# Kernel tuning notes

Measured on AMD Instinct MI355X. Metric: run time of the kernel, lower is better.

## Reference

```python
import jax, jax.numpy as jnp
import numpy as np

KH, KW, STRIDE, PAD, DIL = 3, 3, 1, 1, 1


def setup_inputs() -> dict:
    key = jax.random.key(0)
    ks = jax.random.split(key, 4)
    B, C, H, W, O = 4, 256, 64, 64, 256
    K = KH * KW
    x = jax.random.normal(ks[0], (B, C, H, W), jnp.float32)
    # offset/mask conv params (original inits to zero; use small random so offsets are non-trivial)
    w_om = jax.random.normal(ks[1], (3 * K, C, KH, KW), jnp.float32) * 0.01
    b_om = jnp.zeros((3 * K,), jnp.float32)
    # main weight: kaiming_uniform_(a=1) -> gain = sqrt(2/(1+1^2)) = 1, bound = sqrt(3)/sqrt(fan_in)
    fan_in = C * K
    bound = float(np.sqrt(3.0) / np.sqrt(fan_in))
    weight = jax.random.uniform(ks[2], (O, C, KH, KW), jnp.float32, -bound, bound)
    bias = jnp.zeros((O,), jnp.float32)
    return {"x": x, "w_om": w_om, "b_om": b_om, "weight": weight, "bias": bias}


def _deform_conv2d(x, offset, mask, weight, bias):
    # torchvision.ops.deform_conv2d semantics, deformable_groups=1, stride=1, pad=1, dil=1
    B, C, H, W = x.shape
    K = KH * KW
    # torchvision offset layout: per-tap interleaved (y, x) pairs along channel dim
    off_y = offset[:, 0::2]  # [B, K, H, W]
    off_x = offset[:, 1::2]  # [B, K, H, W]
    ky = (jnp.repeat(jnp.arange(KH), KW) * DIL).astype(x.dtype)  # [K]
    kx = (jnp.tile(jnp.arange(KW), KH) * DIL).astype(x.dtype)    # [K]
    base_y = (jnp.arange(H) * STRIDE - PAD).astype(x.dtype)
    base_x = (jnp.arange(W) * STRIDE - PAD).astype(x.dtype)
    py = base_y[None, None, :, None] + ky[None, :, None, None] + off_y  # [B,K,H,W]
    px = base_x[None, None, None, :] + kx[None, :, None, None] + off_x  # [B,K,H,W]
    y0 = jnp.floor(py)
    x0 = jnp.floor(px)
    ly = py - y0
    lx = px - x0
    y0i = y0.astype(jnp.int32)
    x0i = x0.astype(jnp.int32)
    x_flat = x.reshape(B, C, H * W)

    def gather(yy, xx):
        # zero-padded gather of one bilinear corner -> [B, C, K, H, W]
        valid = ((yy >= 0) & (yy < H) & (xx >= 0) & (xx < W)).astype(x.dtype)
        idx = (jnp.clip(yy, 0, H - 1) * W + jnp.clip(xx, 0, W - 1)).reshape(B, -1)
        g = jax.vmap(lambda xf, i: jnp.take(xf, i, axis=1))(x_flat, idx)
        return g.reshape(B, C, K, H, W) * valid.reshape(B, 1, K, H, W)

    w00 = ((1 - ly) * (1 - lx))[:, None]
    w01 = ((1 - ly) * lx)[:, None]
    w10 = (ly * (1 - lx))[:, None]
    w11 = (ly * lx)[:, None]
    val = (gather(y0i, x0i) * w00 + gather(y0i, x0i + 1) * w01
           + gather(y0i + 1, x0i) * w10 + gather(y0i + 1, x0i + 1) * w11)
    cols = val * mask[:, None]  # modulated columns [B,C,K,H,W]
    out = jnp.einsum('bckhw,ock->bohw', cols, weight.reshape(weight.shape[0], C, K))
    return out + bias[None, :, None, None]


def reference(x, w_om, b_om, weight, bias):
    om = jax.lax.conv_general_dilated(
        x, w_om, (STRIDE, STRIDE), ((PAD, PAD), (PAD, PAD)),
        rhs_dilation=(DIL, DIL), dimension_numbers=('NCHW', 'OIHW', 'NCHW'),
    ) + b_om[None, :, None, None]
    K = KH * KW
    o1, o2, m = om[:, :K], om[:, K:2 * K], om[:, 2 * K:]
    offset = jnp.concatenate([o1, o2], axis=1)  # [B, 2K, H, W]
    mask = jax.nn.sigmoid(m)                    # [B, K, H, W]
    return _deform_conv2d(x, offset, mask, weight, bias)
```

## Files before the change

### kernel.cpp

```cpp
#include <hip/hip_runtime.h>
#include <stdint.h>

#define B_ 4
#define C_ 256
#define H_ 64
#define W_ 64
#define O_ 256
#define K_ 9
#define CK 2304
#define HW 4096
#define NTOT 16384

typedef __bf16 bf16x8 __attribute__((ext_vector_type(8)));
typedef __bf16 bf16x4 __attribute__((ext_vector_type(4)));
typedef float f32x4 __attribute__((ext_vector_type(4)));
typedef float f32x2 __attribute__((ext_vector_type(2)));
typedef f32x2 __attribute__((aligned(4))) f32x2u;

__device__ __forceinline__ uint16_t f2bf(float f) {
  uint32_t u = __builtin_bit_cast(uint32_t, f);
  return (uint16_t)((u + 0x7FFFu + ((u >> 16) & 1u)) >> 16);
}

__device__ __forceinline__ uint32_t pk_bf16(float a, float b) {
  uint16_t lo = __builtin_bit_cast(uint16_t, (__bf16)a);
  uint16_t hi = __builtin_bit_cast(uint16_t, (__bf16)b);
  return (uint32_t)lo | ((uint32_t)hi << 16);
}

__global__ void kA_prep(const float* __restrict__ weight, const float* __restrict__ w_om,
                        const float* __restrict__ x, uint16_t* __restrict__ wb,
                        uint16_t* __restrict__ womb, uint16_t* __restrict__ xT) {
  int bx = blockIdx.x;
  int t = threadIdx.x;
  if (bx < 2304) {
    int idx = bx * 256 + t;
    int o = idx / CK;
    int rem = idx - o * CK;
    int k = rem >> 8, c = rem & 255;
    wb[idx] = f2bf(weight[(o * C_ + c) * K_ + k]);
  } else if (bx < 2592) {
    int idx = (bx - 2304) * 256 + t;
    int j = idx / CK;
    int ck = idx - j * CK;
    int k = ck >> 8, c = ck & 255;
    womb[idx] = (j < 27) ? f2bf(w_om[(j * 256 + c) * 9 + k]) : (uint16_t)0;
  } else {
    int bxl = bx - 2592;
    int ct = bxl & 3;
    int hwt = (bxl >> 2) & 63;
    int b = bxl >> 8;
    int l = t & 63;
    int cq = t >> 6;

    __shared__ __align__(16) uint16_t tile[64 * 72];

    const float* xb = x + ((b * 256 + ct * 64) * HW) + hwt * 64;
#pragma unroll
    for (int i = 0; i < 16; ++i) {
      int c = cq * 16 + i;
      tile[l * 72 + c] = f2bf(xb[c * HW + l]);
    }
    __syncthreads();

    int hw = t >> 2;
    int c8 = (t & 3) * 8;
    uint16_t* dst = xT + ((size_t)b << 20) + (size_t)(hwt * 64 + hw) * 256 + ct * 64;
    *(uint4*)&dst[c8] = *(const uint4*)&tile[hw * 72 + c8];
    *(uint4*)&dst[c8 + 32] = *(const uint4*)&tile[hw * 72 + c8 + 32];
  }
}

__device__ __forceinline__ void write_om(float v, int j, int n, const float* __restrict__ b_om,
                                         float* __restrict__ pypxmk) {
  if (j >= 27) return;
  float s = v + b_om[j];
  int b = n >> 12, hw = n & 4095;
  int h = hw >> 6, w = hw & 63;
  if (j < 18) {
    int k = j >> 1;
    int off = (b * 9 + k) * HW + hw;
    if ((j & 1) == 0)
      pypxmk[off] = (float)(h - 1 + k / 3) + s;
    else
      pypxmk[147456 + off] = (float)(w - 1 + k % 3) + s;
  } else {
    int k = j - 18;
    pypxmk[294912 + (b * 9 + k) * HW + hw] = 1.f / (1.f + __expf(-s));
  }
}

__global__ void k1_mfma(const uint16_t* __restrict__ womb, const uint16_t* __restrict__ xT,
                        const float* __restrict__ b_om, float* __restrict__ pypxmk) {
  int nt = blockIdx.x;
  int t = threadIdx.x;
  int lane = t & 63;
  int wid = t >> 6;
  int lr = lane & 15, q = lane >> 4;
  int n = nt * 64 + wid * 16 + lr;
  int b = n >> 12;
  int hw = n & 4095;
  int y = hw >> 6, xx = hw & 63;
  const uint16_t* xb = xT + ((size_t)b << 20);
  const uint16_t* zrow = womb + 31 * CK;

  f32x4 acc0 = {0.f, 0.f, 0.f, 0.f};
  f32x4 acc1 = {0.f, 0.f, 0.f, 0.f};

#pragma unroll
  for (int k = 0; k < 9; ++k) {
    int dy = k / 3, dx = k - dy * 3;
    int ny = y + dy - 1, nx = xx + dx - 1;
    bool valid = ((unsigned)ny < 64u) && ((unsigned)nx < 64u);
    int row = (min(max(ny, 0), 63) << 6) + min(max(nx, 0), 63);
    const uint16_t* bp = valid ? (xb + row * 256 + q * 8) : (zrow + q * 8);
    const uint16_t* ap = womb + lr * CK + k * 256 + q * 8;
#pragma unroll
    for (int kt = 0; kt < 8; ++kt) {
      int c0 = kt * 32;
      bf16x8 bF = *(const bf16x8*)&bp[c0];
      bf16x8 aF0 = *(const bf16x8*)&ap[c0];
      bf16x8 aF1 = *(const bf16x8*)&ap[16 * CK + c0];
      acc0 = __builtin_amdgcn_mfma_f32_16x16x32_bf16(aF0, bF, acc0, 0, 0, 0);
      acc1 = __builtin_amdgcn_mfma_f32_16x16x32_bf16(aF1, bF, acc1, 0, 0, 0);
    }
  }

#pragma unroll
  for (int r = 0; r < 4; ++r) {
    write_om(acc0[r], q * 4 + r, n, b_om, pypxmk);
    write_om(acc1[r], 16 + q * 4 + r, n, b_om, pypxmk);
  }
}

__global__ void k2_cols(const uint16_t* __restrict__ xT, const float* __restrict__ pypxmk,
                        uint16_t* __restrict__ cols) {
  int bx = blockIdx.x;
  int g = __builtin_amdgcn_readfirstlane(threadIdx.x >> 6);
  int lane = threadIdx.x & 63;

  const float* pyA = pypxmk;
  const float* pxA = pypxmk + 147456;
  const float* mkA = pypxmk + 294912;

  float py_c, px_c, mk_c;
  {
    int p = g;
    int pn = p / 9;
    int k = p - pn * 9;
    int n = (bx << 3) + pn;
    int poff = ((n >> 12) * 9 + k) * HW + (n & 4095);
    py_c = pyA[poff];
    px_c = pxA[poff];
    mk_c = mkA[poff];
  }

  for (int it = 0; it < 18; ++it) {
    int p = it * 4 + g;
    int pn = p / 9;
    int k = p - pn * 9;
    int n = (bx << 3) + pn;
    int b = n >> 12;

    float py = py_c, px = px_c, mk = mk_c;
    if (it < 17) {
      int p2 = (it + 1) * 4 + g;
      int pn2 = p2 / 9;
      int k2 = p2 - pn2 * 9;
      int n2 = (bx << 3) + pn2;
      int poff2 = ((n2 >> 12) * 9 + k2) * HW + (n2 & 4095);
      py_c = pyA[poff2];
      px_c = pxA[poff2];
      mk_c = mkA[poff2];
    }

    float fy0 = floorf(py), fx0 = floorf(px);
    float ly = py - fy0, lx = px - fx0;
    int y0 = (int)fy0, x0 = (int)fx0;
    bool vy0 = ((unsigned)y0 < 64u), vy1 = ((unsigned)(y0 + 1) < 64u);
    bool vx0 = ((unsigned)x0 < 64u), vx1 = ((unsigned)(x0 + 1) < 64u);
    float w00 = (vy0 && vx0) ? (1.f - ly) * (1.f - lx) * mk : 0.f;
    float w01 = (vy0 && vx1) ? (1.f - ly) * lx * mk : 0.f;
    float w10 = (vy1 && vx0) ? ly * (1.f - lx) * mk : 0.f;
    float w11 = (vy1 && vx1) ? ly * lx * mk : 0.f;
    bool sel0 = (x0 >= 63);
    bool sel1 = (x0 >= 0);
    float wa0 = (sel0 ? 0.f : w00) + (sel1 ? 0.f : w01);
    float wb0 = (sel0 ? w00 : 0.f) + (sel1 ? w01 : 0.f);
    float wa1 = (sel0 ? 0.f : w10) + (sel1 ? 0.f : w11);
    float wb1 = (sel0 ? w10 : 0.f) + (sel1 ? w11 : 0.f);
    int bx0 = min(max(x0, 0), 62);
    int a0 = min(max(y0, 0), 63) * 64 + bx0;
    int a1 = min(max(y0 + 1, 0), 63) * 64 + bx0;

    const uint16_t* xb = xT + ((size_t)b << 20);
    bf16x4 r00 = *(const bf16x4*)&xb[a0 * 256 + lane * 4];
    bf16x4 r01 = *(const bf16x4*)&xb[a0 * 256 + 256 + lane * 4];
    bf16x4 r10 = *(const bf16x4*)&xb[a1 * 256 + lane * 4];
    bf16x4 r11 = *(const bf16x4*)&xb[a1 * 256 + 256 + lane * 4];

    float v[4];
#pragma unroll
    for (int i = 0; i < 4; ++i)
      v[i] = wa0 * (float)r00[i] + wb0 * (float)r01[i] +
             wa1 * (float)r10[i] + wb1 * (float)r11[i];

    uint2 pk;
    pk.x = pk_bf16(v[0], v[1]);
    pk.y = pk_bf16(v[2], v[3]);
    *(uint2*)&cols[(size_t)n * CK + k * 256 + lane * 4] = pk;
  }
}

__global__ void k3_gemm(const uint16_t* __restrict__ wb, const uint16_t* __restrict__ cols,
                        const float* __restrict__ bias, float* __restrict__ out) {
  int bx = blockIdx.x;
  int mt = bx & 1;
  int nt = bx >> 1;
  int o0 = mt * 128;
  int n0 = nt * 64;
  int t = threadIdx.x;
  int lane = t & 63;
  int wid = t >> 6;
  int wm = wid >> 1, wn = wid & 1;
  int lr = lane & 15, q = lane >> 4;

  __shared__ __align__(16) uint16_t As[128 * 32];
  __shared__ __align__(16) uint16_t Bs[64 * 32];

  f32x4 acc[4][2];
  const f32x4 zero = {0.f, 0.f, 0.f, 0.f};
#pragma unroll
  for (int i = 0; i < 4; ++i)
#pragma unroll
    for (int j = 0; j < 2; ++j) acc[i][j] = zero;

  int r0 = t >> 2;
  int koff = (t & 3) * 8;
  const uint16_t* gA = wb + (o0 + r0) * CK + koff;
  const uint16_t* gB = cols + (n0 + r0) * CK + koff;

  for (int kt = 0; kt < 72; ++kt) {
    int k0 = kt * 32;
    __builtin_amdgcn_global_load_lds(
        (const __attribute__((address_space(1))) uint32_t*)(gA + k0),
        (__attribute__((address_space(3))) uint32_t*)&As[t * 8], 16, 0, 0);
    __builtin_amdgcn_global_load_lds(
        (const __attribute__((address_space(1))) uint32_t*)(gA + 64 * CK + k0),
        (__attribute__((address_space(3))) uint32_t*)&As[2048 + t * 8], 16, 0, 0);
    __builtin_amdgcn_global_load_lds(
        (const __attribute__((address_space(1))) uint32_t*)(gB + k0),
        (__attribute__((address_space(3))) uint32_t*)&Bs[t * 8], 16, 0, 0);
    __syncthreads();

    bf16x8 aF[4], bF[2];
#pragma unroll
    for (int i = 0; i < 4; ++i)
      aF[i] = *(const bf16x8*)&As[(wm * 64 + i * 16 + lr) * 32 + q * 8];
#pragma unroll
    for (int j = 0; j < 2; ++j)
      bF[j] = *(const bf16x8*)&Bs[(wn * 32 + j * 16 + lr) * 32 + q * 8];
#pragma unroll
    for (int i = 0; i < 4; ++i)
#pragma unroll
      for (int j = 0; j < 2; ++j)
        acc[i][j] = __builtin_amdgcn_mfma_f32_16x16x32_bf16(aF[i], bF[j], acc[i][j], 0, 0, 0);
    __syncthreads();
  }

  int bb = n0 >> 12;
  int hw0 = n0 & 4095;
#pragma unroll
  for (int i = 0; i < 4; ++i) {
#pragma unroll
    for (int r = 0; r < 4; ++r) {
      int o = o0 + wm * 64 + i * 16 + q * 4 + r;
      float bv = bias[o];
      float* orow = out + (bb * O_ + o) * HW + hw0;
#pragma unroll
      for (int j = 0; j < 2; ++j) orow[wn * 32 + j * 16 + lr] = acc[i][j][r] + bv;
    }
  }
}

__global__ void k0_wconv(const float* __restrict__ weight, uint16_t* __restrict__ wb) {
  int idx = blockIdx.x * 256 + threadIdx.x;
  if (idx >= O_ * CK) return;
  int o = idx / CK;
  int rem = idx - o * CK;
  int k = rem >> 8;
  int c = rem & 255;
  wb[idx] = f2bf(weight[(o * C_ + c) * K_ + k]);
}

__global__ void k1_offconv(const float* __restrict__ x, const float* __restrict__ w_om,
                           const float* __restrict__ b_om, float* __restrict__ pypxmk) {
  int bx = blockIdx.x;
  int jq = bx % 7;
  int h = (bx / 7) % H_;
  int b = bx / (7 * H_);
  int t = threadIdx.x;
  int w = t & 63;
  int cs = __builtin_amdgcn_readfirstlane(t >> 6);

  float acc[4] = {0.f, 0.f, 0.f, 0.f};
  const float* xb = x + (b * C_) * HW;

  for (int ci = 0; ci < 64; ++ci) {
    int c = cs * 64 + ci;
    const float* xr = xb + c * HW;
    float xv[3][3];
#pragma unroll
    for (int r = 0; r < 3; ++r) {
      int y = h - 1 + r;
      bool yv = ((unsigned)y < 64u);
#pragma unroll
      for (int dx = 0; dx < 3; ++dx) {
        int xx = w - 1 + dx;
        bool v = yv && ((unsigned)xx < 64u);
        xv[r][dx] = v ? xr[y * 64 + xx] : 0.f;
      }
    }
    const float* wp = w_om + ((jq * 4) * C_ + c) * 9;
#pragma unroll
    for (int jj = 0; jj < 4; ++jj) {
      int j = jq * 4 + jj;
      int jeff = (j < 27) ? jj : 0;
      const float* wj = wp + jeff * (C_ * 9);
      float a = 0.f;
#pragma unroll
      for (int r = 0; r < 3; ++r)
#pragma unroll
        for (int dx = 0; dx < 3; ++dx)
          a = fmaf(xv[r][dx], wj[r * 3 + dx], a);
      acc[jj] += a;
    }
  }

  __shared__ float red[4][4][64];
#pragma unroll
  for (int jj = 0; jj < 4; ++jj) red[cs][jj][w] = acc[jj];
  __syncthreads();

  int jj = t >> 6;
  int j = jq * 4 + jj;
  if (j < 27) {
    float s = red[0][jj][w] + red[1][jj][w] + red[2][jj][w] + red[3][jj][w] + b_om[j];
    float* pyA = pypxmk;
    float* pxA = pypxmk + 147456;
    float* mkA = pypxmk + 294912;
    if (j < 18) {
      int k = j >> 1;
      int off = (b * 9 + k) * HW + h * 64 + w;
      if ((j & 1) == 0)
        pyA[off] = (float)(h - 1 + k / 3) + s;
      else
        pxA[off] = (float)(w - 1 + k % 3) + s;
    } else {
      int k = j - 18;
      mkA[(b * 9 + k) * HW + h * 64 + w] = 1.f / (1.f + __expf(-s));
    }
  }
}

__global__ void k2_fb(const float* __restrict__ x, const float* __restrict__ pypxmk,
                      uint16_t* __restrict__ cols) {
  int bx = blockIdx.x;
  int cg = bx & 15;
  int h = (bx >> 4) & 63;
  int b = bx >> 10;
  int t = threadIdx.x;
  int w = t & 63;
  int g = t >> 6;

  const float* pyA = pypxmk;
  const float* pxA = pypxmk + 147456;
  const float* mkA = pypxmk + 294912;

  __shared__ uint16_t tile[64 * 146];
  const float* xb = x + b * C_ * HW;
  int cbase = cg * 16 + g * 4;

#pragma unroll
  for (int k = 0; k < 9; ++k) {
    int poff = (b * 9 + k) * HW + h * 64 + w;
    float py = pyA[poff];
    float px = pxA[poff];
    float mk = mkA[poff];
    float fy0 = floorf(py), fx0 = floorf(px);
    float ly = py - fy0, lx = px - fx0;
    int y0 = (int)fy0, x0 = (int)fx0;
    bool vy0 = ((unsigned)y0 < 64u), vy1 = ((unsigned)(y0 + 1) < 64u);
    bool vx0 = ((unsigned)x0 < 64u), vx1 = ((unsigned)(x0 + 1) < 64u);
    float w00 = (vy0 && vx0) ? (1.f - ly) * (1.f - lx) * mk : 0.f;
    float w01 = (vy0 && vx1) ? (1.f - ly) * lx * mk : 0.f;
    float w10 = (vy1 && vx0) ? ly * (1.f - lx) * mk : 0.f;
    float w11 = (vy1 && vx1) ? ly * lx * mk : 0.f;
    bool sel0 = (x0 >= 63);
    bool sel1 = (x0 >= 0);
    float wa0 = (sel0 ? 0.f : w00) + (sel1 ? 0.f : w01);
    float wb0 = (sel0 ? w00 : 0.f) + (sel1 ? w01 : 0.f);
    float wa1 = (sel0 ? 0.f : w10) + (sel1 ? 0.f : w11);
    float wb1 = (sel0 ? w10 : 0.f) + (sel1 ? w11 : 0.f);
    int bx0 = min(max(x0, 0), 62);
    int a0 = min(max(y0, 0), 63) * 64 + bx0;
    int a1 = min(max(y0 + 1, 0), 63) * 64 + bx0;

#pragma unroll
    for (int cp = 0; cp < 2; ++cp) {
      const float* xcA = xb + (cbase + cp * 2) * HW;
      const float* xcB = xcA + HW;
      f32x2 A0 = *(const f32x2u*)&xcA[a0];
      f32x2 A1 = *(const f32x2u*)&xcA[a1];
      f32x2 B0 = *(const f32x2u*)&xcB[a0];
      f32x2 B1 = *(const f32x2u*)&xcB[a1];
      float rA = wa0 * A0.x + wb0 * A0.y + wa1 * A1.x + wb1 * A1.y;
      float rB = wa0 * B0.x + wb0 * B0.y + wa1 * B1.x + wb1 * B1.y;
      *(uint32_t*)&tile[w * 146 + k * 16 + g * 4 + cp * 2] = pk_bf16(rA, rB);
    }
  }
  __syncthreads();

#pragma unroll
  for (int it = 0; it < 18; ++it) {
    int u = t + it * 256;
    int wu = u / 72;
    int rem = u - wu * 72;
    int k = rem >> 3;
    int cd = rem & 7;
    uint32_t val = *(const uint32_t*)&tile[wu * 146 + rem * 2];
    int n = b * HW + h * 64 + wu;
    int dst = n * CK + k * 256 + cg * 16 + cd * 2;
    *(uint32_t*)&cols[dst] = val;
  }
}

__global__ void k3_flex(const uint16_t* __restrict__ wb, const uint16_t* __restrict__ cols,
                        const float* __restrict__ bias, float* __restrict__ out) {
  int bx = blockIdx.x;
  int mt = bx & 1;
  int nt = bx >> 1;
  int o0 = mt * 128;
  int n0 = nt * 128;
  int t = threadIdx.x;
  int lane = t & 63;
  int wid = t >> 6;
  int wm = wid >> 1, wn = wid & 1;
  int lr = lane & 15, q = lane >> 4;

  __shared__ __align__(16) uint16_t As[128 * 32];
  __shared__ __align__(16) uint16_t Bs[128 * 32];

  f32x4 acc[4][4];
  const f32x4 zero = {0.f, 0.f, 0.f, 0.f};
#pragma unroll
  for (int i = 0; i < 4; ++i)
#pragma unroll
    for (int j = 0; j < 4; ++j) acc[i][j] = zero;

  int r0 = t >> 2;
  int koff = (t & 3) * 8;
  const uint16_t* gA = wb + (o0 + r0) * CK + koff;
  const uint16_t* gB = cols + (n0 + r0) * CK + koff;

  for (int kt = 0; kt < 72; ++kt) {
    int k0 = kt * 32;
    __builtin_amdgcn_global_load_lds(
        (const __attribute__((address_space(1))) uint32_t*)(gA + k0),
        (__attribute__((address_space(3))) uint32_t*)&As[t * 8], 16, 0, 0);
    __builtin_amdgcn_global_load_lds(
        (const __attribute__((address_space(1))) uint32_t*)(gA + 64 * CK + k0),
        (__attribute__((address_space(3))) uint32_t*)&As[2048 + t * 8], 16, 0, 0);
    __builtin_amdgcn_global_load_lds(
        (const __attribute__((address_space(1))) uint32_t*)(gB + k0),
        (__attribute__((address_space(3))) uint32_t*)&Bs[t * 8], 16, 0, 0);
    __builtin_amdgcn_global_load_lds(
        (const __attribute__((address_space(1))) uint32_t*)(gB + 64 * CK + k0),
        (__attribute__((address_space(3))) uint32_t*)&Bs[2048 + t * 8], 16, 0, 0);
    __syncthreads();

    bf16x8 aF[4], bF[4];
#pragma unroll
    for (int i = 0; i < 4; ++i)
      aF[i] = *(const bf16x8*)&As[(wm * 64 + i * 16 + lr) * 32 + q * 8];
#pragma unroll
    for (int j = 0; j < 4; ++j)
      bF[j] = *(const bf16x8*)&Bs[(wn * 64 + j * 16 + lr) * 32 + q * 8];
#pragma unroll
    for (int i = 0; i < 4; ++i)
#pragma unroll
      for (int j = 0; j < 4; ++j)
        acc[i][j] = __builtin_amdgcn_mfma_f32_16x16x32_bf16(aF[i], bF[j], acc[i][j], 0, 0, 0);
    __syncthreads();
  }

  int bb = n0 >> 12;
  int hw0 = n0 & 4095;
#pragma unroll
  for (int i = 0; i < 4; ++i) {
#pragma unroll
    for (int r = 0; r < 4; ++r) {
      int o = o0 + wm * 64 + i * 16 + q * 4 + r;
      float bv = bias[o];
      float* orow = out + (bb * O_ + o) * HW + hw0;
#pragma unroll
      for (int j = 0; j < 4; ++j) orow[wn * 64 + j * 16 + lr] = acc[i][j][r] + bv;
    }
  }
}

extern "C" void kernel_launch(void* const* d_in, const int* in_sizes, int n_in,
                              void* d_out, int out_size, void* d_ws, size_t ws_size,
                              hipStream_t stream) {
  const float* x = (const float*)d_in[0];
  const float* w_om = (const float*)d_in[1];
  const float* b_om = (const float*)d_in[2];
  const float* weight = (const float*)d_in[3];
  const float* bias = (const float*)d_in[4];
  float* out = (float*)d_out;

  char* ws = (char*)d_ws;
  uint16_t* wb = (uint16_t*)ws;
  uint16_t* womb = (uint16_t*)(ws + 1179648);
  uint16_t* xT = (uint16_t*)(ws + 1327104);
  float* pypxmk = (float*)(ws + 9715712);
  uint16_t* cols = (uint16_t*)(ws + 11485184);

  if (ws_size >= 86982656ull) {
    hipLaunchKernelGGL(kA_prep, dim3(3616), dim3(256), 0, stream, weight, w_om, x, wb, womb, xT);
    hipLaunchKernelGGL(k1_mfma, dim3(256), dim3(256), 0, stream, womb, xT, b_om, pypxmk);
    hipLaunchKernelGGL(k2_cols, dim3(2048), dim3(256), 0, stream, xT, pypxmk, cols);
    hipLaunchKernelGGL(k3_gemm, dim3(512), dim3(256), 0, stream, wb, cols, bias, out);
  } else {
    float* pypx_fb = (float*)(ws + 1179648);
    uint16_t* colsf = (uint16_t*)(ws + 2949120);
    hipLaunchKernelGGL(k0_wconv, dim3(2304), dim3(256), 0, stream, weight, wb);
    hipLaunchKernelGGL(k1_offconv, dim3(4 * 64 * 7), dim3(256), 0, stream, x, w_om, b_om, pypx_fb);
    hipLaunchKernelGGL(k2_fb, dim3(4 * 64 * 16), dim3(256), 0, stream, x, pypx_fb, colsf);
    hipLaunchKernelGGL(k3_flex, dim3(256), dim3(256), 0, stream, wb, colsf, bias, out);
  }
}
```

Measured before the change: 173.7 us.

## Fuse deformable gather into GEMM, building column tiles in LDS

Replaces the separate column-building kernel and GEMM with one fused kernel. Each block gathers bilinear-interpolated, mask-weighted columns for one kernel tap into an XOR-swizzled LDS slab, then runs MFMA over all 256 output channels while double-buffering weight tiles through LDS. This removes the write and re-read of the large bf16 column buffer in global memory and one launch. In exchange the gather is serialized with the MMA per tap, there are only 256 blocks of 512 threads, and the workspace threshold changes.

```diff
diff --git a/kernel.cpp b/kernel.cpp
--- a/kernel.cpp
+++ b/kernel.cpp
@@ -133,47 +133,24 @@
   }
 }
 
-__global__ void k2_cols(const uint16_t* __restrict__ xT, const float* __restrict__ pypxmk,
-                        uint16_t* __restrict__ cols) {
-  int bx = blockIdx.x;
-  int g = __builtin_amdgcn_readfirstlane(threadIdx.x >> 6);
-  int lane = threadIdx.x & 63;
-
-  const float* pyA = pypxmk;
-  const float* pxA = pypxmk + 147456;
-  const float* mkA = pypxmk + 294912;
-
-  float py_c, px_c, mk_c;
-  {
-    int p = g;
-    int pn = p / 9;
-    int k = p - pn * 9;
-    int n = (bx << 3) + pn;
-    int poff = ((n >> 12) * 9 + k) * HW + (n & 4095);
-    py_c = pyA[poff];
-    px_c = pxA[poff];
-    mk_c = mkA[poff];
-  }
-
-  for (int it = 0; it < 18; ++it) {
-    int p = it * 4 + g;
-    int pn = p / 9;
-    int k = p - pn * 9;
-    int n = (bx << 3) + pn;
-    int b = n >> 12;
-
-    float py = py_c, px = px_c, mk = mk_c;
-    if (it < 17) {
-      int p2 = (it + 1) * 4 + g;
-      int pn2 = p2 / 9;
-      int k2 = p2 - pn2 * 9;
-      int n2 = (bx << 3) + pn2;
-      int poff2 = ((n2 >> 12) * 9 + k2) * HW + (n2 & 4095);
-      py_c = pyA[poff2];
-      px_c = pxA[poff2];
-      mk_c = mkA[poff2];
-    }
-
+
+struct GatherState {
+  float wa0[4], wb0[4], wa1[4], wb1[4];
+  bf16x4 r00[4], r01[4], r10[4], r11[4];
+};
+
+__device__ __forceinline__ void gather_issue(GatherState& S, const uint16_t* __restrict__ xb,
+                                             const float* __restrict__ pyA,
+                                             const float* __restrict__ pxA,
+                                             const float* __restrict__ mkA,
+                                             int b, int kg, int n0, int rbase, int lane) {
+#pragma unroll
+  for (int j = 0; j < 4; ++j) {
+    int nrow = rbase + j;
+    int poff = (b * 9 + kg) * HW + ((n0 + nrow) & 4095);
+    float py = pyA[poff];
+    float px = pxA[poff];
+    float mk = mkA[poff];
     float fy0 = floorf(py), fx0 = floorf(px);
     float ly = py - fy0, lx = px - fx0;
     int y0 = (int)fy0, x0 = (int)fx0;
@@ -185,48 +162,99 @@
     float w11 = (vy1 && vx1) ? ly * lx * mk : 0.f;
     bool sel0 = (x0 >= 63);
     bool sel1 = (x0 >= 0);
-    float wa0 = (sel0 ? 0.f : w00) + (sel1 ? 0.f : w01);
-    float wb0 = (sel0 ? w00 : 0.f) + (sel1 ? w01 : 0.f);
-    float wa1 = (sel0 ? 0.f : w10) + (sel1 ? 0.f : w11);
-    float wb1 = (sel0 ? w10 : 0.f) + (sel1 ? w11 : 0.f);
+    S.wa0[j] = (sel0 ? 0.f : w00) + (sel1 ? 0.f : w01);
+    S.wb0[j] = (sel0 ? w00 : 0.f) + (sel1 ? w01 : 0.f);
+    S.wa1[j] = (sel0 ? 0.f : w10) + (sel1 ? 0.f : w11);
+    S.wb1[j] = (sel0 ? w10 : 0.f) + (sel1 ? w11 : 0.f);
     int bx0 = min(max(x0, 0), 62);
     int a0 = min(max(y0, 0), 63) * 64 + bx0;
     int a1 = min(max(y0 + 1, 0), 63) * 64 + bx0;
-
-    const uint16_t* xb = xT + ((size_t)b << 20);
-    bf16x4 r00 = *(const bf16x4*)&xb[a0 * 256 + lane * 4];
-    bf16x4 r01 = *(const bf16x4*)&xb[a0 * 256 + 256 + lane * 4];
-    bf16x4 r10 = *(const bf16x4*)&xb[a1 * 256 + lane * 4];
-    bf16x4 r11 = *(const bf16x4*)&xb[a1 * 256 + 256 + lane * 4];
-
+    S.r00[j] = *(const bf16x4*)&xb[a0 * 256 + lane * 4];
+    S.r01[j] = *(const bf16x4*)&xb[a0 * 256 + 256 + lane * 4];
+    S.r10[j] = *(const bf16x4*)&xb[a1 * 256 + lane * 4];
+    S.r11[j] = *(const bf16x4*)&xb[a1 * 256 + 256 + lane * 4];
+  }
+}
+
+__device__ __forceinline__ void gather_finish(const GatherState& S, uint16_t* bslab,
+                                              int rbase, int lane) {
+#pragma unroll
+  for (int j = 0; j < 4; ++j) {
+    int nrow = rbase + j;
     float v[4];
 #pragma unroll
     for (int i = 0; i < 4; ++i)
-      v[i] = wa0 * (float)r00[i] + wb0 * (float)r01[i] +
-             wa1 * (float)r10[i] + wb1 * (float)r11[i];
-
+      v[i] = S.wa0[j] * (float)S.r00[j][i] + S.wb0[j] * (float)S.r01[j][i] +
+             S.wa1[j] * (float)S.r10[j][i] + S.wb1[j] * (float)S.r11[j][i];
     uint2 pk;
     pk.x = pk_bf16(v[0], v[1]);
     pk.y = pk_bf16(v[2], v[3]);
-    *(uint2*)&cols[(size_t)n * CK + k * 256 + lane * 4] = pk;
-  }
-}
-
-__global__ void k3_gemm(const uint16_t* __restrict__ wb, const uint16_t* __restrict__ cols,
-                        const float* __restrict__ bias, float* __restrict__ out) {
-  int bx = blockIdx.x;
-  int mt = bx & 1;
-  int nt = bx >> 1;
-  int o0 = mt * 128;
-  int n0 = nt * 64;
+    int chunk = lane >> 1;
+    int chs = (chunk & 24) | ((chunk & 7) ^ (nrow & 7));
+    *(uint2*)&bslab[nrow * 256 + chs * 8 + (lane & 1) * 4] = pk;
+  }
+}
+
+__device__ __forceinline__ void stageA(const uint16_t* __restrict__ wb, uint16_t* asbuf,
+                                       int kbase, int t) {
+#pragma unroll
+  for (int i = 0; i < 4; ++i) {
+    int rr = i * 64 + (t >> 3);
+    const uint16_t* src = wb + rr * CK + kbase + (((t & 7) ^ (rr & 7)) << 3);
+    __builtin_amdgcn_global_load_lds(
+        (const __attribute__((address_space(1))) uint32_t*)src,
+        (__attribute__((address_space(3))) uint32_t*)&asbuf[i * 4096 + t * 8], 16, 0, 0);
+  }
+}
+
+__device__ __forceinline__ void mma_step(const uint16_t* AsP, const uint16_t* BsP,
+                                         f32x4 acc[4][2], int wm, int wn, int lr, int q,
+                                         int kt2) {
+#pragma unroll
+  for (int kc = 0; kc < 2; ++kc) {
+    bf16x8 aF[4], bF[2];
+#pragma unroll
+    for (int i = 0; i < 4; ++i) {
+      int row = wm * 64 + i * 16 + lr;
+      aF[i] = *(const bf16x8*)&AsP[row * 64 + (((kc * 4 + q) ^ (row & 7)) << 3)];
+    }
+#pragma unroll
+    for (int j = 0; j < 2; ++j) {
+      int row = wn * 32 + j * 16 + lr;
+      int kidx = kt2 * 8 + kc * 4 + q;
+      int chs = (kidx & 24) | ((kidx & 7) ^ (row & 7));
+      bF[j] = *(const bf16x8*)&BsP[row * 256 + chs * 8];
+    }
+#pragma unroll
+    for (int i = 0; i < 4; ++i)
+#pragma unroll
+      for (int j = 0; j < 2; ++j)
+        acc[i][j] = __builtin_amdgcn_mfma_f32_16x16x32_bf16(aF[i], bF[j], acc[i][j], 0, 0, 0);
+  }
+}
+
+__global__ __launch_bounds__(512, 2) void k23_fused(const uint16_t* __restrict__ wb,
+                                                    const uint16_t* __restrict__ xT,
+                                                    const float* __restrict__ pypxmk,
+                                                    const float* __restrict__ bias,
+                                                    float* __restrict__ out) {
+  __shared__ __align__(16) uint16_t As[2][16384];
+  __shared__ __align__(16) uint16_t Bs[16384];
+
   int t = threadIdx.x;
   int lane = t & 63;
-  int wid = t >> 6;
+  int wid = __builtin_amdgcn_readfirstlane(t >> 6);
+  int lr = lane & 15, q = lane >> 4;
   int wm = wid >> 1, wn = wid & 1;
-  int lr = lane & 15, q = lane >> 4;
-
-  __shared__ __align__(16) uint16_t As[128 * 32];
-  __shared__ __align__(16) uint16_t Bs[64 * 32];
+  int bx = blockIdx.x;
+  int swz = (bx & 7) * 32 + (bx >> 3);
+  int n0 = swz * 64;
+  int b = n0 >> 12;
+  int hw0 = n0 & 4095;
+  const uint16_t* xb = xT + ((size_t)b << 20);
+  const float* pyA = pypxmk;
+  const float* pxA = pypxmk + 147456;
+  const float* mkA = pypxmk + 294912;
 
   f32x4 acc[4][2];
   const f32x4 zero = {0.f, 0.f, 0.f, 0.f};
@@ -235,48 +263,41 @@
 #pragma unroll
     for (int j = 0; j < 2; ++j) acc[i][j] = zero;
 
-  int r0 = t >> 2;
-  int koff = (t & 3) * 8;
-  const uint16_t* gA = wb + (o0 + r0) * CK + koff;
-  const uint16_t* gB = cols + (n0 + r0) * CK + koff;
-
-  for (int kt = 0; kt < 72; ++kt) {
-    int k0 = kt * 32;
-    __builtin_amdgcn_global_load_lds(
-        (const __attribute__((address_space(1))) uint32_t*)(gA + k0),
-        (__attribute__((address_space(3))) uint32_t*)&As[t * 8], 16, 0, 0);
-    __builtin_amdgcn_global_load_lds(
-        (const __attribute__((address_space(1))) uint32_t*)(gA + 64 * CK + k0),
-        (__attribute__((address_space(3))) uint32_t*)&As[2048 + t * 8], 16, 0, 0);
-    __builtin_amdgcn_global_load_lds(
-        (const __attribute__((address_space(1))) uint32_t*)(gB + k0),
-        (__attribute__((address_space(3))) uint32_t*)&Bs[t * 8], 16, 0, 0);
-    __syncthreads();
-
-    bf16x8 aF[4], bF[2];
-#pragma unroll
-    for (int i = 0; i < 4; ++i)
-      aF[i] = *(const bf16x8*)&As[(wm * 64 + i * 16 + lr) * 32 + q * 8];
-#pragma unroll
-    for (int j = 0; j < 2; ++j)
-      bF[j] = *(const bf16x8*)&Bs[(wn * 32 + j * 16 + lr) * 32 + q * 8];
-#pragma unroll
-    for (int i = 0; i < 4; ++i)
-#pragma unroll
-      for (int j = 0; j < 2; ++j)
-        acc[i][j] = __builtin_amdgcn_mfma_f32_16x16x32_bf16(aF[i], bF[j], acc[i][j], 0, 0, 0);
-    __syncthreads();
-  }
-
-  int bb = n0 >> 12;
-  int hw0 = n0 & 4095;
+  GatherState S;
+  int wrow = wid * 8;
+
+  gather_issue(S, xb, pyA, pxA, mkA, b, 0, n0, wrow, lane);
+  gather_finish(S, Bs, wrow, lane);
+  gather_issue(S, xb, pyA, pxA, mkA, b, 0, n0, wrow + 4, lane);
+  gather_finish(S, Bs, wrow + 4, lane);
+  stageA(wb, As[0], 0, t);
+  __syncthreads();
+
+  for (int k = 0; k < 9; ++k) {
+    for (int kt2 = 0; kt2 < 4; ++kt2) {
+      if (!(k == 8 && kt2 == 3)) {
+        int kb2 = (kt2 == 3) ? (k + 1) * 256 : k * 256 + (kt2 + 1) * 64;
+        stageA(wb, As[(kt2 + 1) & 1], kb2, t);
+      }
+      mma_step(As[kt2 & 1], Bs, acc, wm, wn, lr, q, kt2);
+      __syncthreads();
+    }
+    if (k < 8) {
+      gather_issue(S, xb, pyA, pxA, mkA, b, k + 1, n0, wrow, lane);
+      gather_finish(S, Bs, wrow, lane);
+      gather_issue(S, xb, pyA, pxA, mkA, b, k + 1, n0, wrow + 4, lane);
+      gather_finish(S, Bs, wrow + 4, lane);
+      __syncthreads();
+    }
+  }
+
 #pragma unroll
   for (int i = 0; i < 4; ++i) {
 #pragma unroll
     for (int r = 0; r < 4; ++r) {
-      int o = o0 + wm * 64 + i * 16 + q * 4 + r;
+      int o = wm * 64 + i * 16 + q * 4 + r;
       float bv = bias[o];
-      float* orow = out + (bb * O_ + o) * HW + hw0;
+      float* orow = out + (b * O_ + o) * HW + hw0;
 #pragma unroll
       for (int j = 0; j < 2; ++j) orow[wn * 32 + j * 16 + lr] = acc[i][j][r] + bv;
     }
@@ -524,13 +545,11 @@
   uint16_t* womb = (uint16_t*)(ws + 1179648);
   uint16_t* xT = (uint16_t*)(ws + 1327104);
   float* pypxmk = (float*)(ws + 9715712);
-  uint16_t* cols = (uint16_t*)(ws + 11485184);
-
-  if (ws_size >= 86982656ull) {
+
+  if (ws_size >= 11485184ull) {
     hipLaunchKernelGGL(kA_prep, dim3(3616), dim3(256), 0, stream, weight, w_om, x, wb, womb, xT);
     hipLaunchKernelGGL(k1_mfma, dim3(256), dim3(256), 0, stream, womb, xT, b_om, pypxmk);
-    hipLaunchKernelGGL(k2_cols, dim3(2048), dim3(256), 0, stream, xT, pypxmk, cols);
-    hipLaunchKernelGGL(k3_gemm, dim3(512), dim3(256), 0, stream, wb, cols, bias, out);
+    hipLaunchKernelGGL(k23_fused, dim3(256), dim3(512), 0, stream, wb, xT, pypxmk, bias, out);
   } else {
     float* pypx_fb = (float*)(ws + 1179648);
     uint16_t* colsf = (uint16_t*)(ws + 2949120);
```

Measured after the change: 168.9 us. -2.8%, faster.
